# Kernel optimization log

Measured on AMD Instinct MI355X. Metric: run time of the kernel, lower is better.

The kernel has to match this reference:

```python
import jax, jax.numpy as jnp
import numpy as np

EPS = 1e-12  # torch F.normalize default eps

def _l2_normalize(x):
    # F.normalize(x, dim=1): x / max(||x||_2, eps), per row
    n = jnp.linalg.norm(x, axis=1, keepdims=True)
    return x / jnp.maximum(n, EPS)

def setup_inputs() -> dict:
    key = jax.random.key(0)
    ks = jax.random.split(key, 7)
    B, D = 8192, 4096
    s = 1.0 / np.sqrt(D)  # keep activations well-scaled like nn.Linear init
    return {
        "x":  jax.random.normal(ks[0], (B, D), dtype=jnp.float32),
        "W0": jax.random.normal(ks[1], (D, D), dtype=jnp.float32) * s,
        "b0": jax.random.normal(ks[2], (D,),   dtype=jnp.float32) * s,
        "W1": jax.random.normal(ks[3], (D, D), dtype=jnp.float32) * s,
        "b1": jax.random.normal(ks[4], (D,),   dtype=jnp.float32) * s,
        "W2": jax.random.normal(ks[5], (D, D), dtype=jnp.float32) * s,
        "b2": jax.random.normal(ks[6], (D,),   dtype=jnp.float32) * s,
    }

def reference(x, W0, b0, W1, b1, W2, b2):
    # per layer: out = relu(Linear(l2_normalize(x, dim=1))); collect all layer outputs
    params = [(W0, b0), (W1, b1), (W2, b2)]
    outs = []
    h = x
    for W, b in params:
        hn = _l2_normalize(h)
        # nn.Linear stores weight as [out, in]: y = hn @ W.T + b
        h = jax.nn.relu(jnp.einsum('bi,oi->bo', hn, W) + b)
        outs.append(h)
    return tuple(outs)
```

## Files before the change

### kernel.cpp

```cpp
#include <hip/hip_runtime.h>
#include <hip/hip_bf16.h>


#define NROWS 8192
#define DIM   4096

typedef __bf16 bf16x8 __attribute__((ext_vector_type(8)));
typedef float  f32x4  __attribute__((ext_vector_type(4)));

__device__ static inline short f2bf(float f) {
  __hip_bfloat16 h = __float2bfloat16(f);
  return __builtin_bit_cast(short, h);
}

#define BARRIER() do { asm volatile("" ::: "memory"); \
                       __builtin_amdgcn_s_barrier();  \
                       asm volatile("" ::: "memory"); } while (0)
#define GATE()   do { asm volatile("s_waitcnt lgkmcnt(0)" ::: "memory"); \
                      __builtin_amdgcn_sched_barrier(0); } while (0)

__global__ __launch_bounds__(512, 2)
void gemm256_bias_relu(const short* __restrict__ A,
                       const short* __restrict__ Bw,
                       const float* __restrict__ bias,
                       float* __restrict__ C,
                       int M, int N, int K)
{
  __shared__ short lds[4][16384];

  int bid = blockIdx.x;
  const int nwg = gridDim.x;
  if ((nwg & 7) == 0) { const int cpx = nwg >> 3; bid = (bid & 7) * cpx + (bid >> 3); }
  const int nbn  = N >> 8;
  const int brow = (bid / nbn) << 8;
  const int bcol = (bid % nbn) << 8;

  const int lane = threadIdx.x & 63;
  const int wid  = __builtin_amdgcn_readfirstlane(threadIdx.x >> 6);
  const int wr   = wid >> 2;
  const int wc   = wid & 3;

  float bv[4];
#pragma unroll
  for (int j = 0; j < 4; ++j)
    bv[j] = bias[bcol + wc * 64 + j * 16 + (lane & 15)];

  f32x4 acc[8][4] = {};

  const size_t rowK = (size_t)K * 2;
  char* const  ldsB = (char*)&lds[0][0];

  const int r8  = lane >> 3;
  const int kcs = (lane & 7) ^ r8;
  const char* AgL = (const char*)A  + (size_t)(brow + r8) * rowK + (size_t)kcs * 16;
  const char* BgL = (const char*)Bw + (size_t)(bcol + r8) * rowK + (size_t)kcs * 16;
  int rbo[4], rbb[4];
#pragma unroll
  for (int i = 0; i < 4; ++i) {
    const int rb = wid * 8 + i * 64;
    rbo[i] = rb * (int)rowK;
    rbb[i] = rb * 128;
  }

  auto stage_half = [&](int parity, int op, int h, int tile) {
    const char* gp = (op ? BgL : AgL) + ((size_t)tile << 7);
    char* lb = ldsB + (parity * 2 + op) * 32768;
#pragma unroll
    for (int s = 0; s < 2; ++s) {
      const int idx = h * 2 + s;
      __builtin_amdgcn_global_load_lds(
          (const __attribute__((address_space(1))) void*)(gp + rbo[idx]),
          (__attribute__((address_space(3))) void*)(lb + rbb[idx]), 16, 0, 0);
    }
  };

  const int l15  = lane & 15;
  const int xlo  = ((lane >> 4) ^ (lane & 3)) * 16;
  const int b2   = (lane >> 2) & 1;
  const int k64[2] = { b2 << 6, (1 - b2) << 6 };
  const int abase = (wr * 128 + l15) * 128 + xlo;
  const int bbase = (wc * 64  + l15) * 128 + xlo;

  const int NT = K >> 6;

  bf16x8 aX[4][2], aY[4][2], bF[4][2];

#define LOAD_FRAG(DST, PTR, BASE, I0)                                        \
  _Pragma("unroll")                                                          \
  for (int ii = 0; ii < 4; ++ii)                                             \
    _Pragma("unroll")                                                        \
    for (int ks = 0; ks < 2; ++ks)                                           \
      DST[ii][ks] = *reinterpret_cast<const bf16x8*>(                        \
          (PTR) + (BASE) + ((I0) + ii) * 2048 + k64[ks]);

#define MFMA16(I0, AF)                                                       \
  _Pragma("unroll")                                                          \
  for (int ks = 0; ks < 2; ++ks)                                             \
    _Pragma("unroll")                                                        \
    for (int ii = 0; ii < 4; ++ii)                                           \
      _Pragma("unroll")                                                      \
      for (int j = 0; j < 4; ++j)                                            \
        acc[(I0) + ii][j] = __builtin_amdgcn_mfma_f32_16x16x32_bf16(         \
            AF[ii][ks], bF[j][ks], acc[(I0) + ii][j], 0, 0, 0);

  stage_half(0, 0, 0, 0); stage_half(0, 0, 1, 0);
  stage_half(0, 1, 0, 0); stage_half(0, 1, 1, 0);
  if (NT > 1) { stage_half(1, 1, 0, 1); stage_half(1, 1, 1, 1); }
  if (NT > 1) asm volatile("s_waitcnt vmcnt(4)" ::: "memory");
  else        asm volatile("s_waitcnt vmcnt(0)" ::: "memory");
  BARRIER();
  LOAD_FRAG(aX, ldsB, abase, 0)

  for (int t = 0; t < NT; ++t) {
    const int cur = t & 1, nxt = cur ^ 1;
    const char* At = ldsB + (cur * 2 + 0) * 32768;
    const char* Bt = ldsB + (cur * 2 + 1) * 32768;
    const char* An = ldsB + (nxt * 2 + 0) * 32768;

    if (t + 1 < NT) { stage_half(nxt, 0, 0, t + 1); stage_half(nxt, 0, 1, t + 1); }
    LOAD_FRAG(bF, Bt, bbase, 0)
    BARRIER();
    GATE();
    LOAD_FRAG(aY, At, abase, 4)
    __builtin_amdgcn_s_setprio(1);
    MFMA16(0, aX)
    __builtin_amdgcn_s_setprio(0);

    asm volatile("s_waitcnt vmcnt(0)" ::: "memory");
    BARRIER();
    GATE();
    if (t + 2 < NT) { stage_half(cur, 1, 0, t + 2); stage_half(cur, 1, 1, t + 2); }
    if (t + 1 < NT) { LOAD_FRAG(aX, An, abase, 0) }
    __builtin_amdgcn_s_setprio(1);
    MFMA16(4, aY)
    __builtin_amdgcn_s_setprio(0);
  }
#undef MFMA16
#undef LOAD_FRAG

#pragma unroll
  for (int i = 0; i < 8; ++i) {
    const int rbase = brow + wr * 128 + i * 16 + ((lane >> 4) << 2);
#pragma unroll
    for (int j = 0; j < 4; ++j) {
      const int col = bcol + wc * 64 + j * 16 + (lane & 15);
#pragma unroll
      for (int r = 0; r < 4; ++r) {
        const float v = acc[i][j][r] + bv[j];
        C[(size_t)(rbase + r) * N + col] = v > 0.f ? v : 0.f;
      }
    }
  }
}

__global__ __launch_bounds__(256)
void rownorm_bf16(const float* __restrict__ in, short* __restrict__ out)
{
  const int row = blockIdx.x;
  const int t0  = threadIdx.x;
  const float4* inr = (const float4*)(in + (size_t)row * DIM);

  float4 v[4];
  float ss = 0.f;
#pragma unroll
  for (int t = 0; t < 4; ++t) {
    v[t] = inr[t0 + t * 256];
    ss += v[t].x * v[t].x + v[t].y * v[t].y + v[t].z * v[t].z + v[t].w * v[t].w;
  }
#pragma unroll
  for (int off = 32; off > 0; off >>= 1)
    ss += __shfl_down(ss, off, 64);

  __shared__ float wss[4];
  if ((t0 & 63) == 0) wss[t0 >> 6] = ss;
  __syncthreads();
  const float tot   = wss[0] + wss[1] + wss[2] + wss[3];
  const float scale = 1.f / fmaxf(sqrtf(tot), 1e-12f);

  short4* outr = (short4*)(out + (size_t)row * DIM);
#pragma unroll
  for (int t = 0; t < 4; ++t) {
    short4 o;
    o.x = f2bf(v[t].x * scale);
    o.y = f2bf(v[t].y * scale);
    o.z = f2bf(v[t].z * scale);
    o.w = f2bf(v[t].w * scale);
    outr[t0 + t * 256] = o;
  }
}

__global__ __launch_bounds__(256)
void cast_bf16(const float* __restrict__ in, short* __restrict__ out, int n4)
{
  int i = blockIdx.x * 256 + threadIdx.x;
  const int stride = gridDim.x * 256;
  for (; i < n4; i += stride) {
    const float4 v = ((const float4*)in)[i];
    short4 o;
    o.x = f2bf(v.x);
    o.y = f2bf(v.y);
    o.z = f2bf(v.z);
    o.w = f2bf(v.w);
    ((short4*)out)[i] = o;
  }
}

extern "C" void kernel_launch(void* const* d_in, const int* in_sizes, int n_in,
                              void* d_out, int out_size, void* d_ws, size_t ws_size,
                              hipStream_t stream) {
  const float* x = (const float*)d_in[0];
  const float* W[3]    = { (const float*)d_in[1], (const float*)d_in[3], (const float*)d_in[5] };
  const float* bias[3] = { (const float*)d_in[2], (const float*)d_in[4], (const float*)d_in[6] };
  float* out = (float*)d_out;

  short* hn = (short*)d_ws;
  short* Wb = (short*)((char*)d_ws + (size_t)NROWS * DIM * 2);

  const size_t layer_elems = (size_t)NROWS * DIM;
  const float* hin = x;

  for (int L = 0; L < 3; ++L) {
    cast_bf16<<<2048, 256, 0, stream>>>(W[L], Wb, DIM * DIM / 4);
    rownorm_bf16<<<NROWS, 256, 0, stream>>>(hin, hn);
    gemm256_bias_relu<<<(NROWS / 256) * (DIM / 256), 512, 0, stream>>>(
        hn, Wb, bias[L], out + (size_t)L * layer_elems, NROWS, DIM, DIM);
    hin = out + (size_t)L * layer_elems;
  }
}
```

Before: 779.2 us.

## Pre-tile weights into MFMA fragment order and load B directly from global

The weight cast kernel now writes bf16 weights in a layout that matches the MFMA B-fragment order, so each lane reads its 16-byte fragment contiguously. The GEMM no longer stages B through LDS. It loads B fragments straight from global memory into registers, halves LDS use to A-only double buffering, and restructures the inner loop into four MFMA quarters that interleave the B loads. The aim is to cut LDS traffic and barrier pressure, at the cost of more global load latency exposed to each wave and uncached reuse of B across the waves that share it.

```diff
diff --git a/kernel.cpp b/kernel.cpp
--- a/kernel.cpp
+++ b/kernel.cpp
@@ -7,6 +7,7 @@
 
 typedef __bf16 bf16x8 __attribute__((ext_vector_type(8)));
 typedef float  f32x4  __attribute__((ext_vector_type(4)));
+typedef short  short8 __attribute__((ext_vector_type(8)));
 
 __device__ static inline short f2bf(float f) {
   __hip_bfloat16 h = __float2bfloat16(f);
@@ -18,15 +19,17 @@
                        asm volatile("" ::: "memory"); } while (0)
 #define GATE()   do { asm volatile("s_waitcnt lgkmcnt(0)" ::: "memory"); \
                       __builtin_amdgcn_sched_barrier(0); } while (0)
+#define VMW(N)   do { asm volatile("s_waitcnt vmcnt(" #N ")" ::: "memory"); \
+                      __builtin_amdgcn_sched_barrier(0); } while (0)
 
 __global__ __launch_bounds__(512, 2)
 void gemm256_bias_relu(const short* __restrict__ A,
-                       const short* __restrict__ Bw,
+                       const short* __restrict__ Wt,
                        const float* __restrict__ bias,
                        float* __restrict__ C,
                        int M, int N, int K)
 {
-  __shared__ short lds[4][16384];
+  __shared__ short lds[2][16384];
 
   int bid = blockIdx.x;
   const int nwg = gridDim.x;
@@ -36,15 +39,10 @@
   const int bcol = (bid % nbn) << 8;
 
   const int lane = threadIdx.x & 63;
-  const int wid  = __builtin_amdgcn_readfirstlane(threadIdx.x >> 6);
+  const int wid  = threadIdx.x >> 6;
   const int wr   = wid >> 2;
   const int wc   = wid & 3;
 
-  float bv[4];
-#pragma unroll
-  for (int j = 0; j < 4; ++j)
-    bv[j] = bias[bcol + wc * 64 + j * 16 + (lane & 15)];
-
   f32x4 acc[8][4] = {};
 
   const size_t rowK = (size_t)K * 2;
@@ -52,8 +50,7 @@
 
   const int r8  = lane >> 3;
   const int kcs = (lane & 7) ^ r8;
-  const char* AgL = (const char*)A  + (size_t)(brow + r8) * rowK + (size_t)kcs * 16;
-  const char* BgL = (const char*)Bw + (size_t)(bcol + r8) * rowK + (size_t)kcs * 16;
+  const char* AgL = (const char*)A + (size_t)(brow + r8) * rowK + (size_t)kcs * 16;
   int rbo[4], rbb[4];
 #pragma unroll
   for (int i = 0; i < 4; ++i) {
@@ -61,17 +58,14 @@
     rbo[i] = rb * (int)rowK;
     rbb[i] = rb * 128;
   }
-
-  auto stage_half = [&](int parity, int op, int h, int tile) {
-    const char* gp = (op ? BgL : AgL) + ((size_t)tile << 7);
-    char* lb = ldsB + (parity * 2 + op) * 32768;
-#pragma unroll
-    for (int s = 0; s < 2; ++s) {
-      const int idx = h * 2 + s;
+  auto stage_A = [&](int parity, int tile) {
+    const char* gp = AgL + ((size_t)tile << 7);
+    char* lb = ldsB + parity * 32768;
+#pragma unroll
+    for (int s = 0; s < 4; ++s)
       __builtin_amdgcn_global_load_lds(
-          (const __attribute__((address_space(1))) void*)(gp + rbo[idx]),
-          (__attribute__((address_space(3))) void*)(lb + rbb[idx]), 16, 0, 0);
-    }
+          (const __attribute__((address_space(1))) void*)(gp + rbo[s]),
+          (__attribute__((address_space(3))) void*)(lb + rbb[s]), 16, 0, 0);
   };
 
   const int l15  = lane & 15;
@@ -79,65 +73,85 @@
   const int b2   = (lane >> 2) & 1;
   const int k64[2] = { b2 << 6, (1 - b2) << 6 };
   const int abase = (wr * 128 + l15) * 128 + xlo;
-  const int bbase = (wc * 64  + l15) * 128 + xlo;
+
+  const int KB = K >> 5;
+  const int nbase = (bcol >> 4) + wc * 4;
+  const char* pB0 = (const char*)Wt + ((size_t)(nbase + 0) * KB * 64 + lane) * 16;
+  const char* pB1 = (const char*)Wt + ((size_t)(nbase + 1) * KB * 64 + lane) * 16;
+  const char* pB2 = (const char*)Wt + ((size_t)(nbase + 2) * KB * 64 + lane) * 16;
+  const char* pB3 = (const char*)Wt + ((size_t)(nbase + 3) * KB * 64 + lane) * 16;
 
   const int NT = K >> 6;
 
-  bf16x8 aX[4][2], aY[4][2], bF[4][2];
-
-#define LOAD_FRAG(DST, PTR, BASE, I0)                                        \
+  bf16x8 aX[4][2], aY[4][2], b01[2][2], b23[2][2];
+
+#define LOAD_AF(DST, PTR, I0)                                                \
   _Pragma("unroll")                                                          \
   for (int ii = 0; ii < 4; ++ii)                                             \
     _Pragma("unroll")                                                        \
     for (int ks = 0; ks < 2; ++ks)                                           \
       DST[ii][ks] = *reinterpret_cast<const bf16x8*>(                        \
-          (PTR) + (BASE) + ((I0) + ii) * 2048 + k64[ks]);
-
-#define MFMA16(I0, AF)                                                       \
+          (PTR) + abase + ((I0) + ii) * 2048 + k64[ks]);
+
+#define LOAD_BP(DST, PJ0, PJ1, TOFF)                                         \
+  DST[0][0] = *reinterpret_cast<const bf16x8*>((PJ0) + (TOFF));              \
+  DST[0][1] = *reinterpret_cast<const bf16x8*>((PJ0) + (TOFF) + 1024);       \
+  DST[1][0] = *reinterpret_cast<const bf16x8*>((PJ1) + (TOFF));              \
+  DST[1][1] = *reinterpret_cast<const bf16x8*>((PJ1) + (TOFF) + 1024);
+
+#define MFMA16(I0, AF, J0, BF)                                               \
   _Pragma("unroll")                                                          \
   for (int ks = 0; ks < 2; ++ks)                                             \
     _Pragma("unroll")                                                        \
     for (int ii = 0; ii < 4; ++ii)                                           \
       _Pragma("unroll")                                                      \
-      for (int j = 0; j < 4; ++j)                                            \
-        acc[(I0) + ii][j] = __builtin_amdgcn_mfma_f32_16x16x32_bf16(         \
-            AF[ii][ks], bF[j][ks], acc[(I0) + ii][j], 0, 0, 0);
-
-  stage_half(0, 0, 0, 0); stage_half(0, 0, 1, 0);
-  stage_half(0, 1, 0, 0); stage_half(0, 1, 1, 0);
-  if (NT > 1) { stage_half(1, 1, 0, 1); stage_half(1, 1, 1, 1); }
-  if (NT > 1) asm volatile("s_waitcnt vmcnt(4)" ::: "memory");
-  else        asm volatile("s_waitcnt vmcnt(0)" ::: "memory");
+      for (int jj = 0; jj < 2; ++jj)                                         \
+        acc[(I0) + ii][(J0) + jj] = __builtin_amdgcn_mfma_f32_16x16x32_bf16( \
+            AF[ii][ks], BF[jj][ks], acc[(I0) + ii][(J0) + jj], 0, 0, 0);
+
+  stage_A(0, 0);
+  LOAD_BP(b01, pB0, pB1, 0)
+  VMW(0);
   BARRIER();
-  LOAD_FRAG(aX, ldsB, abase, 0)
+  LOAD_AF(aX, ldsB, 0)
 
   for (int t = 0; t < NT; ++t) {
-    const int cur = t & 1, nxt = cur ^ 1;
-    const char* At = ldsB + (cur * 2 + 0) * 32768;
-    const char* Bt = ldsB + (cur * 2 + 1) * 32768;
-    const char* An = ldsB + (nxt * 2 + 0) * 32768;
-
-    if (t + 1 < NT) { stage_half(nxt, 0, 0, t + 1); stage_half(nxt, 0, 1, t + 1); }
-    LOAD_FRAG(bF, Bt, bbase, 0)
+    const int cur = t & 1;
+    const char* At = ldsB + cur * 32768;
+    const char* An = ldsB + (cur ^ 1) * 32768;
+    const size_t toff = (size_t)t << 11;
+
+    LOAD_BP(b23, pB2, pB3, toff)
+    if (t + 1 < NT) { stage_A(cur ^ 1, t + 1); VMW(8); }
+    else            { VMW(4); }
+    GATE();
+    LOAD_AF(aY, At, 4)
+    __builtin_amdgcn_s_setprio(1);
+    MFMA16(0, aX, 0, b01)
+    __builtin_amdgcn_s_setprio(0);
+    GATE();
+    __builtin_amdgcn_s_setprio(1);
+    MFMA16(4, aY, 0, b01)
+    __builtin_amdgcn_s_setprio(0);
+    VMW(0);
     BARRIER();
-    GATE();
-    LOAD_FRAG(aY, At, abase, 4)
-    __builtin_amdgcn_s_setprio(1);
-    MFMA16(0, aX)
-    __builtin_amdgcn_s_setprio(0);
-
-    asm volatile("s_waitcnt vmcnt(0)" ::: "memory");
-    BARRIER();
-    GATE();
-    if (t + 2 < NT) { stage_half(cur, 1, 0, t + 2); stage_half(cur, 1, 1, t + 2); }
-    if (t + 1 < NT) { LOAD_FRAG(aX, An, abase, 0) }
-    __builtin_amdgcn_s_setprio(1);
-    MFMA16(4, aY)
+    if (t + 1 < NT) { LOAD_BP(b01, pB0, pB1, toff + 2048) }
+    __builtin_amdgcn_s_setprio(1);
+    MFMA16(0, aX, 2, b23)
+    __builtin_amdgcn_s_setprio(0);
+    if (t + 1 < NT) { LOAD_AF(aX, An, 0) }
+    __builtin_amdgcn_s_setprio(1);
+    MFMA16(4, aY, 2, b23)
     __builtin_amdgcn_s_setprio(0);
   }
 #undef MFMA16
-#undef LOAD_FRAG
-
+#undef LOAD_AF
+#undef LOAD_BP
+
+  float bv[4];
+#pragma unroll
+  for (int j = 0; j < 4; ++j)
+    bv[j] = bias[bcol + wc * 64 + j * 16 + (lane & 15)];
 #pragma unroll
   for (int i = 0; i < 8; ++i) {
     const int rbase = brow + wr * 128 + i * 16 + ((lane >> 4) << 2);
@@ -190,18 +204,26 @@
 }
 
 __global__ __launch_bounds__(256)
-void cast_bf16(const float* __restrict__ in, short* __restrict__ out, int n4)
+void cast_w_tiled(const float* __restrict__ in, short* __restrict__ out,
+                  int N, int K)
 {
+  const int KB = K >> 5;
+  const int total = (N >> 4) * KB * 64;
   int i = blockIdx.x * 256 + threadIdx.x;
   const int stride = gridDim.x * 256;
-  for (; i < n4; i += stride) {
-    const float4 v = ((const float4*)in)[i];
-    short4 o;
-    o.x = f2bf(v.x);
-    o.y = f2bf(v.y);
-    o.z = f2bf(v.z);
-    o.w = f2bf(v.w);
-    ((short4*)out)[i] = o;
+  for (; i < total; i += stride) {
+    const int l  = i & 63;
+    const int f  = i >> 6;
+    const int kb = f % KB;
+    const int nb = f / KB;
+    const int row = nb * 16 + (l & 15);
+    const int k0  = kb * 32 + (l >> 4) * 8;
+    const float4 v0 = *(const float4*)(in + (size_t)row * K + k0);
+    const float4 v1 = *(const float4*)(in + (size_t)row * K + k0 + 4);
+    short8 o;
+    o[0] = f2bf(v0.x); o[1] = f2bf(v0.y); o[2] = f2bf(v0.z); o[3] = f2bf(v0.w);
+    o[4] = f2bf(v1.x); o[5] = f2bf(v1.y); o[6] = f2bf(v1.z); o[7] = f2bf(v1.w);
+    *reinterpret_cast<short8*>(out + (size_t)i * 8) = o;
   }
 }
 
@@ -214,16 +236,16 @@
   float* out = (float*)d_out;
 
   short* hn = (short*)d_ws;
-  short* Wb = (short*)((char*)d_ws + (size_t)NROWS * DIM * 2);
+  short* Wt = (short*)((char*)d_ws + (size_t)NROWS * DIM * 2);
 
   const size_t layer_elems = (size_t)NROWS * DIM;
   const float* hin = x;
 
   for (int L = 0; L < 3; ++L) {
-    cast_bf16<<<2048, 256, 0, stream>>>(W[L], Wb, DIM * DIM / 4);
+    cast_w_tiled<<<2048, 256, 0, stream>>>(W[L], Wt, DIM, DIM);
     rownorm_bf16<<<NROWS, 256, 0, stream>>>(hin, hn);
     gemm256_bias_relu<<<(NROWS / 256) * (DIM / 256), 512, 0, stream>>>(
-        hn, Wb, bias[L], out + (size_t)L * layer_elems, NROWS, DIM, DIM);
+        hn, Wt, bias[L], out + (size_t)L * layer_elems, NROWS, DIM, DIM);
     hin = out + (size_t)L * layer_elems;
   }
 }
```

After: 832.0 us. 6.8% more time.

## Triple-buffer A tiles in LDS to prefetch two K-steps ahead

Applied to the files above, without the earlier changes.

The GEMM kernel grows LDS from four to five 32 KB buffers, giving A a three-slot ring and B a double buffer, so A loads are issued two tiles ahead and waits become partial (vmcnt(4)) rather than full drains. The aim is to hide more global-memory latency behind the MFMA work. The bias load is moved after the main loop to free registers, and the wave id is no longer forced scalar. The extra LDS (160 KB per block) may break the two-blocks-per-CU occupancy the launch bounds ask for, and the rotating buffer pointers may add address arithmetic.

```diff
diff --git a/kernel.cpp b/kernel.cpp
--- a/kernel.cpp
+++ b/kernel.cpp
@@ -17,6 +17,8 @@
                        __builtin_amdgcn_s_barrier();  \
                        asm volatile("" ::: "memory"); } while (0)
 #define GATE()   do { asm volatile("s_waitcnt lgkmcnt(0)" ::: "memory"); \
+                      __builtin_amdgcn_sched_barrier(0); } while (0)
+#define VMW(N)   do { asm volatile("s_waitcnt vmcnt(" #N ")" ::: "memory"); \
                       __builtin_amdgcn_sched_barrier(0); } while (0)
 
 __global__ __launch_bounds__(512, 2)
@@ -26,7 +28,7 @@
                        float* __restrict__ C,
                        int M, int N, int K)
 {
-  __shared__ short lds[4][16384];
+  __shared__ short lds[5][16384];
 
   int bid = blockIdx.x;
   const int nwg = gridDim.x;
@@ -36,14 +38,9 @@
   const int bcol = (bid % nbn) << 8;
 
   const int lane = threadIdx.x & 63;
-  const int wid  = __builtin_amdgcn_readfirstlane(threadIdx.x >> 6);
+  const int wid  = threadIdx.x >> 6;
   const int wr   = wid >> 2;
   const int wc   = wid & 3;
-
-  float bv[4];
-#pragma unroll
-  for (int j = 0; j < 4; ++j)
-    bv[j] = bias[bcol + wc * 64 + j * 16 + (lane & 15)];
 
   f32x4 acc[8][4] = {};
 
@@ -61,17 +58,13 @@
     rbo[i] = rb * (int)rowK;
     rbb[i] = rb * 128;
   }
-
-  auto stage_half = [&](int parity, int op, int h, int tile) {
-    const char* gp = (op ? BgL : AgL) + ((size_t)tile << 7);
-    char* lb = ldsB + (parity * 2 + op) * 32768;
-#pragma unroll
-    for (int s = 0; s < 2; ++s) {
-      const int idx = h * 2 + s;
+  auto stage = [&](const char* gsrc, char* lb, int tile) {
+    const char* gp = gsrc + ((size_t)tile << 7);
+#pragma unroll
+    for (int s = 0; s < 4; ++s)
       __builtin_amdgcn_global_load_lds(
-          (const __attribute__((address_space(1))) void*)(gp + rbo[idx]),
-          (__attribute__((address_space(3))) void*)(lb + rbb[idx]), 16, 0, 0);
-    }
+          (const __attribute__((address_space(1))) void*)(gp + rbo[s]),
+          (__attribute__((address_space(3))) void*)(lb + rbb[s]), 16, 0, 0);
   };
 
   const int l15  = lane & 15;
@@ -103,41 +96,50 @@
         acc[(I0) + ii][j] = __builtin_amdgcn_mfma_f32_16x16x32_bf16(         \
             AF[ii][ks], bF[j][ks], acc[(I0) + ii][j], 0, 0, 0);
 
-  stage_half(0, 0, 0, 0); stage_half(0, 0, 1, 0);
-  stage_half(0, 1, 0, 0); stage_half(0, 1, 1, 0);
-  if (NT > 1) { stage_half(1, 1, 0, 1); stage_half(1, 1, 1, 1); }
-  if (NT > 1) asm volatile("s_waitcnt vmcnt(4)" ::: "memory");
-  else        asm volatile("s_waitcnt vmcnt(0)" ::: "memory");
+  char* a0 = ldsB;
+  char* a1 = ldsB + 32768;
+  char* a2 = ldsB + 65536;
+  char* b0 = ldsB + 98304;
+  char* b1 = ldsB + 131072;
+
+  stage(AgL, a0, 0);
+  if (NT > 1) stage(AgL, a1, 1);
+  stage(BgL, b0, 0);
+  if (NT > 1) stage(BgL, b1, 1);
+  VMW(0);
   BARRIER();
-  LOAD_FRAG(aX, ldsB, abase, 0)
+  LOAD_FRAG(aX, a0, abase, 0)
 
   for (int t = 0; t < NT; ++t) {
-    const int cur = t & 1, nxt = cur ^ 1;
-    const char* At = ldsB + (cur * 2 + 0) * 32768;
-    const char* Bt = ldsB + (cur * 2 + 1) * 32768;
-    const char* An = ldsB + (nxt * 2 + 0) * 32768;
-
-    if (t + 1 < NT) { stage_half(nxt, 0, 0, t + 1); stage_half(nxt, 0, 1, t + 1); }
-    LOAD_FRAG(bF, Bt, bbase, 0)
+    if (t + 2 < NT) stage(AgL, a2, t + 2);
+    LOAD_FRAG(bF, b0, bbase, 0)
     BARRIER();
     GATE();
-    LOAD_FRAG(aY, At, abase, 4)
+    LOAD_FRAG(aY, a0, abase, 4)
     __builtin_amdgcn_s_setprio(1);
     MFMA16(0, aX)
     __builtin_amdgcn_s_setprio(0);
 
-    asm volatile("s_waitcnt vmcnt(0)" ::: "memory");
+    if (t + 2 < NT) { VMW(4); }
+    else            { VMW(0); }
     BARRIER();
     GATE();
-    if (t + 2 < NT) { stage_half(cur, 1, 0, t + 2); stage_half(cur, 1, 1, t + 2); }
-    if (t + 1 < NT) { LOAD_FRAG(aX, An, abase, 0) }
+    if (t + 2 < NT) stage(BgL, b0, t + 2);
+    if (t + 1 < NT) { LOAD_FRAG(aX, a1, abase, 0) }
     __builtin_amdgcn_s_setprio(1);
     MFMA16(4, aY)
     __builtin_amdgcn_s_setprio(0);
+
+    char* tmp = a0; a0 = a1; a1 = a2; a2 = tmp;
+    char* tb = b0; b0 = b1; b1 = tb;
   }
 #undef MFMA16
 #undef LOAD_FRAG
 
+  float bv[4];
+#pragma unroll
+  for (int j = 0; j < 4; ++j)
+    bv[j] = bias[bcol + wc * 64 + j * 16 + (lane & 15)];
 #pragma unroll
   for (int i = 0; i < 8; ++i) {
     const int rbase = brow + wr * 128 + i * 16 + ((lane >> 4) << 2);
```

Result: slower. 807.8 us (+3.7%).

## Fuse row-norm into GEMM epilogue via deferred scaling and atomic sum-of-squares

Applied to the files above, without the earlier changes.

Row L2 normalization moves out of the separate per-layer rownorm pass. The GEMM now runs on unnormalized bf16 activations and applies the 1/||row|| scale in the epilogue, since scaling commutes with the matmul. The epilogue also writes the next layer's bf16 input and accumulates per-row sums of squares with atomics, which removes an fp32 read pass over the 128MB activation per layer. In exchange it adds extra bf16 stores and atomics in the epilogue and changes the prologue vmcnt wait to a full drain. Atomic ordering makes the results slightly nondeterministic.

```diff
diff --git a/kernel.cpp b/kernel.cpp
--- a/kernel.cpp
+++ b/kernel.cpp
@@ -18,12 +18,17 @@
                        asm volatile("" ::: "memory"); } while (0)
 #define GATE()   do { asm volatile("s_waitcnt lgkmcnt(0)" ::: "memory"); \
                       __builtin_amdgcn_sched_barrier(0); } while (0)
+#define VMW(N)   do { asm volatile("s_waitcnt vmcnt(" #N ")" ::: "memory"); \
+                      __builtin_amdgcn_sched_barrier(0); } while (0)
 
 __global__ __launch_bounds__(512, 2)
 void gemm256_bias_relu(const short* __restrict__ A,
                        const short* __restrict__ Bw,
                        const float* __restrict__ bias,
+                       const float* __restrict__ ssIn,
                        float* __restrict__ C,
+                       float* __restrict__ ssOut,
+                       short* __restrict__ hnOut,
                        int M, int N, int K)
 {
   __shared__ short lds[4][16384];
@@ -106,8 +111,7 @@
   stage_half(0, 0, 0, 0); stage_half(0, 0, 1, 0);
   stage_half(0, 1, 0, 0); stage_half(0, 1, 1, 0);
   if (NT > 1) { stage_half(1, 1, 0, 1); stage_half(1, 1, 1, 1); }
-  if (NT > 1) asm volatile("s_waitcnt vmcnt(4)" ::: "memory");
-  else        asm volatile("s_waitcnt vmcnt(0)" ::: "memory");
+  VMW(0);
   BARRIER();
   LOAD_FRAG(aX, ldsB, abase, 0)
 
@@ -126,7 +130,7 @@
     MFMA16(0, aX)
     __builtin_amdgcn_s_setprio(0);
 
-    asm volatile("s_waitcnt vmcnt(0)" ::: "memory");
+    VMW(0);
     BARRIER();
     GATE();
     if (t + 2 < NT) { stage_half(cur, 1, 0, t + 2); stage_half(cur, 1, 1, t + 2); }
@@ -138,18 +142,76 @@
 #undef MFMA16
 #undef LOAD_FRAG
 
+  const bool aux = (hnOut != nullptr);
 #pragma unroll
   for (int i = 0; i < 8; ++i) {
     const int rbase = brow + wr * 128 + i * 16 + ((lane >> 4) << 2);
 #pragma unroll
-    for (int j = 0; j < 4; ++j) {
-      const int col = bcol + wc * 64 + j * 16 + (lane & 15);
-#pragma unroll
-      for (int r = 0; r < 4; ++r) {
-        const float v = acc[i][j][r] + bv[j];
-        C[(size_t)(rbase + r) * N + col] = v > 0.f ? v : 0.f;
+    for (int r = 0; r < 4; ++r) {
+      const int row = rbase + r;
+      const float s = ssIn ? (1.f / fmaxf(sqrtf(ssIn[row]), 1e-12f)) : 1.f;
+      float ssq = 0.f;
+#pragma unroll
+      for (int j = 0; j < 4; ++j) {
+        const int col = bcol + wc * 64 + j * 16 + l15;
+        float v = fmaf(acc[i][j][r], s, bv[j]);
+        v = v > 0.f ? v : 0.f;
+        C[(size_t)row * N + col] = v;
+        if (aux) {
+          hnOut[(size_t)row * N + col] = f2bf(v);
+          ssq = fmaf(v, v, ssq);
+        }
+      }
+      if (aux) {
+        ssq += __shfl_xor(ssq, 1, 64);
+        ssq += __shfl_xor(ssq, 2, 64);
+        ssq += __shfl_xor(ssq, 4, 64);
+        ssq += __shfl_xor(ssq, 8, 64);
+        if (l15 == 0) atomicAdd(ssOut + row, ssq);
       }
     }
+  }
+}
+
+__global__ __launch_bounds__(256)
+void castrow_bf16(const float* __restrict__ in, short* __restrict__ out,
+                  float* __restrict__ ss0, float* __restrict__ ss1,
+                  float* __restrict__ ss2)
+{
+  const int row = blockIdx.x;
+  const int t0  = threadIdx.x;
+  const float4* inr = (const float4*)(in + (size_t)row * DIM);
+
+  float4 v[4];
+  float ss = 0.f;
+#pragma unroll
+  for (int t = 0; t < 4; ++t) {
+    v[t] = inr[t0 + t * 256];
+    ss += v[t].x * v[t].x + v[t].y * v[t].y + v[t].z * v[t].z + v[t].w * v[t].w;
+  }
+#pragma unroll
+  for (int off = 32; off > 0; off >>= 1)
+    ss += __shfl_down(ss, off, 64);
+
+  __shared__ float wss[4];
+  if ((t0 & 63) == 0) wss[t0 >> 6] = ss;
+  __syncthreads();
+  if (t0 == 0) ss0[row] = wss[0] + wss[1] + wss[2] + wss[3];
+
+  short4* outr = (short4*)(out + (size_t)row * DIM);
+#pragma unroll
+  for (int t = 0; t < 4; ++t) {
+    short4 o;
+    o.x = f2bf(v[t].x);
+    o.y = f2bf(v[t].y);
+    o.z = f2bf(v[t].z);
+    o.w = f2bf(v[t].w);
+    outr[t0 + t * 256] = o;
+  }
+
+  if (row < 64) {
+    if (t0 < 128) ss1[row * 128 + t0] = 0.f;
+    else          ss2[row * 128 + (t0 - 128)] = 0.f;
   }
 }
 
@@ -213,17 +275,41 @@
   const float* bias[3] = { (const float*)d_in[2], (const float*)d_in[4], (const float*)d_in[6] };
   float* out = (float*)d_out;
 
-  short* hn = (short*)d_ws;
-  short* Wb = (short*)((char*)d_ws + (size_t)NROWS * DIM * 2);
-
   const size_t layer_elems = (size_t)NROWS * DIM;
-  const float* hin = x;
-
-  for (int L = 0; L < 3; ++L) {
-    cast_bf16<<<2048, 256, 0, stream>>>(W[L], Wb, DIM * DIM / 4);
-    rownorm_bf16<<<NROWS, 256, 0, stream>>>(hin, hn);
-    gemm256_bias_relu<<<(NROWS / 256) * (DIM / 256), 512, 0, stream>>>(
-        hn, Wb, bias[L], out + (size_t)L * layer_elems, NROWS, DIM, DIM);
-    hin = out + (size_t)L * layer_elems;
-  }
-}
+  const size_t hnB = layer_elems * 2;
+  const size_t needed = hnB * 2 + (size_t)DIM * DIM * 2 + 3 * NROWS * 4;
+  const int ngrid = (NROWS / 256) * (DIM / 256);
+
+  if (ws_size >= needed) {
+    short* hn0 = (short*)d_ws;
+    short* hn1 = (short*)((char*)d_ws + hnB);
+    short* Wb  = (short*)((char*)d_ws + 2 * hnB);
+    float* ss0 = (float*)((char*)d_ws + 2 * hnB + (size_t)DIM * DIM * 2);
+    float* ss1 = ss0 + NROWS;
+    float* ss2 = ss1 + NROWS;
+
+    cast_bf16<<<2048, 256, 0, stream>>>(W[0], Wb, DIM * DIM / 4);
+    castrow_bf16<<<NROWS, 256, 0, stream>>>(x, hn0, ss0, ss1, ss2);
+    gemm256_bias_relu<<<ngrid, 512, 0, stream>>>(
+        hn0, Wb, bias[0], ss0, out, ss1, hn1, NROWS, DIM, DIM);
+    cast_bf16<<<2048, 256, 0, stream>>>(W[1], Wb, DIM * DIM / 4);
+    gemm256_bias_relu<<<ngrid, 512, 0, stream>>>(
+        hn1, Wb, bias[1], ss1, out + layer_elems, ss2, hn0, NROWS, DIM, DIM);
+    cast_bf16<<<2048, 256, 0, stream>>>(W[2], Wb, DIM * DIM / 4);
+    gemm256_bias_relu<<<ngrid, 512, 0, stream>>>(
+        hn0, Wb, bias[2], ss2, out + 2 * layer_elems, nullptr, nullptr,
+        NROWS, DIM, DIM);
+  } else {
+    short* hn = (short*)d_ws;
+    short* Wb = (short*)((char*)d_ws + hnB);
+    const float* hin = x;
+    for (int L = 0; L < 3; ++L) {
+      cast_bf16<<<2048, 256, 0, stream>>>(W[L], Wb, DIM * DIM / 4);
+      rownorm_bf16<<<NROWS, 256, 0, stream>>>(hin, hn);
+      gemm256_bias_relu<<<ngrid, 512, 0, stream>>>(
+          hn, Wb, bias[L], nullptr, out + (size_t)L * layer_elems,
+          nullptr, nullptr, NROWS, DIM, DIM);
+      hin = out + (size_t)L * layer_elems;
+    }
+  }
+}
```

Measured after the change: 840.7 us. 1.08x slower.
